# Kernel tuning notes

Measured on AMD Instinct MI355X. Metric: run time of the kernel, lower is better.

## Reference

```python
import jax, jax.numpy as jnp
import numpy as np


def cmul(a, b):
    # complex multiply on (..., 2) real/imag pairs
    ar, ai = a[..., 0], a[..., 1]
    br, bi = b[..., 0], b[..., 1]
    return jnp.stack([ar * br - ai * bi, ar * bi + ai * br], axis=-1)


def butterfly_apply(x, diag, subdiag, superdiag, k):
    # x: [B, n, 2]; tridiagonal-at-offset-k complex matrix applied to x.
    # diag: [n, 2]; subdiag/superdiag padded to [n, 2], first n-k entries used.
    n = x.shape[-2]
    out = cmul(diag, x)
    out = out.at[..., k:, :].add(cmul(subdiag[: n - k], x[..., : n - k, :]))
    out = out.at[..., : n - k, :].add(cmul(superdiag[: n - k], x[..., k:, :]))
    return out


def block_perm(x, logit, s):
    # Soft block permutation: within each contiguous block of size s,
    # mix identity with even-odd separation (prob p0), then mix each half
    # with its reversal (probs p1, p2). Acts identically on real & imag.
    B, n, _ = x.shape
    p = jax.nn.sigmoid(logit)
    y = x.reshape(B, n // s, s, 2)
    eo = jnp.concatenate([y[:, :, 0::2, :], y[:, :, 1::2, :]], axis=2)
    y = (1 - p[0]) * y + p[0] * eo
    h = s // 2
    first = (1 - p[1]) * y[:, :, :h, :] + p[1] * jnp.flip(y[:, :, :h, :], axis=2)
    second = (1 - p[2]) * y[:, :, h:, :] + p[2] * jnp.flip(y[:, :, h:, :], axis=2)
    return jnp.concatenate([first, second], axis=2).reshape(B, n, 2)


def trifat_forward(x, perm_logits, diags, subdiags, superdiags, bias):
    B, n = x.shape
    depth, m = diags.shape[0], diags.shape[1]
    perm_sizes = [n >> i for i in range(m - 1)][::-1]  # 4, 8, ..., n
    # real_to_complex: zero imaginary part
    xc = jnp.stack([x, jnp.zeros_like(x)], axis=-1)  # [B, n, 2]
    for d in range(depth):
        for j, s in enumerate(perm_sizes):
            xc = block_perm(xc, perm_logits[d, j], s)
        for i in range(m):
            k = n >> (i + 1)  # offsets n/2, n/4, ..., 1
            xc = butterfly_apply(xc, diags[d, i], subdiags[d, i], superdiags[d, i], k)
    return xc[..., 0] + bias  # take real part, add bias


def setup_inputs() -> dict:
    key = jax.random.key(0)
    ks = jax.random.split(key, 6)
    B, n, depth = 4096, 1024, 2
    m = int(np.log2(n))
    return {
        "x": jax.random.normal(ks[0], (B, n), jnp.float32),
        "perm_logits": jax.random.normal(ks[1], (depth, m - 1, 3), jnp.float32),
        "diags": jax.random.normal(ks[2], (depth, m, n, 2), jnp.float32),
        "subdiags": jax.random.normal(ks[3], (depth, m, n, 2), jnp.float32),
        "superdiags": jax.random.normal(ks[4], (depth, m, n, 2), jnp.float32),
        "bias": jnp.zeros((n,), jnp.float32),
    }


def reference(x, perm_logits, diags, subdiags, superdiags, bias):
    return trifat_forward(x, perm_logits, diags, subdiags, superdiags, bias)
```

## Files before the change

### kernel.cpp

```cpp
#include <hip/hip_runtime.h>

#define N 1024
#define THREADS 256
#define EPT 4

__device__ __forceinline__ float2* run_pipeline(
    float2* bufA, float2* bufB, int tid,
    const float* __restrict__ logits,
    const float* __restrict__ diags,
    const float* __restrict__ subd,
    const float* __restrict__ supd)
{
    float2* src = bufA;
    float2* dst = bufB;

    for (int d = 0; d < 2; ++d) {
        for (int j = 0; j < 9; ++j) {
            const int s = 4 << j;
            const int h = s >> 1;
            const float* lg = logits + (d * 9 + j) * 3;
            const float p0 = 1.0f / (1.0f + expf(-lg[0]));
            const float p1 = 1.0f / (1.0f + expf(-lg[1]));
            const float p2 = 1.0f / (1.0f + expf(-lg[2]));
#pragma unroll
            for (int e = 0; e < EPT; ++e) {
                const int idx = tid + e * THREADS;
                const int base = idx & ~(s - 1);
                const int t = idx & (s - 1);
                const bool lo = (t < h);

                const int eo_t = lo ? (2 * t) : (2 * (t - h) + 1);
                const float2 xt  = src[idx];
                const float2 xeo = src[base + eo_t];
                float2 yt;
                yt.x = xt.x + p0 * (xeo.x - xt.x);
                yt.y = xt.y + p0 * (xeo.y - xt.y);

                const int tm = lo ? (h - 1 - t) : (s + h - 1 - t);
                const float psel = lo ? p1 : p2;
                const int eo_m = (tm < h) ? (2 * tm) : (2 * (tm - h) + 1);
                const float2 xm   = src[base + tm];
                const float2 xmeo = src[base + eo_m];
                float2 ym;
                ym.x = xm.x + p0 * (xmeo.x - xm.x);
                ym.y = xm.y + p0 * (xmeo.y - xm.y);

                float2 o;
                o.x = yt.x + psel * (ym.x - yt.x);
                o.y = yt.y + psel * (ym.y - yt.y);
                dst[idx] = o;
            }
            __syncthreads();
            float2* tmp = src; src = dst; dst = tmp;
        }
        for (int i = 0; i < 10; ++i) {
            const int k = N >> (i + 1);
            const float2* Dg = (const float2*)(diags + (size_t)((d * 10 + i) * N) * 2);
            const float2* Sb = (const float2*)(subd  + (size_t)((d * 10 + i) * N) * 2);
            const float2* Sp = (const float2*)(supd  + (size_t)((d * 10 + i) * N) * 2);
#pragma unroll
            for (int e = 0; e < EPT; ++e) {
                const int idx = tid + e * THREADS;
                const float2 xv = src[idx];
                const float2 dg = Dg[idx];
                float2 o;
                o.x = dg.x * xv.x - dg.y * xv.y;
                o.y = dg.x * xv.y + dg.y * xv.x;
                if (idx >= k) {
                    const float2 xs = src[idx - k];
                    const float2 sb = Sb[idx - k];
                    o.x += sb.x * xs.x - sb.y * xs.y;
                    o.y += sb.x * xs.y + sb.y * xs.x;
                }
                if (idx < N - k) {
                    const float2 xp = src[idx + k];
                    const float2 sp = Sp[idx];
                    o.x += sp.x * xp.x - sp.y * xp.y;
                    o.y += sp.x * xp.y + sp.y * xp.x;
                }
                dst[idx] = o;
            }
            __syncthreads();
            float2* tmp = src; src = dst; dst = tmp;
        }
    }
    return src;
}

__global__ __launch_bounds__(THREADS) void trifat_kernel(
    const float* __restrict__ x,
    const float* __restrict__ logits,
    const float* __restrict__ diags,
    const float* __restrict__ supd_unused,
    const float* __restrict__ supd,
    const float* __restrict__ bias,
    float* __restrict__ out,
    int B);

__global__ __launch_bounds__(THREADS) void trifat_kernel_impl(
    const float* __restrict__ x,
    const float* __restrict__ logits,
    const float* __restrict__ diags,
    const float* __restrict__ subd,
    const float* __restrict__ supd,
    const float* __restrict__ bias,
    float* __restrict__ out,
    int B)
{
    __shared__ float2 bufA[N];
    __shared__ float2 bufB[N];

    const int row = blockIdx.x;
    const int tid = threadIdx.x;
    if (row >= B) return;

    const float* xr = x + (size_t)row * N;
#pragma unroll
    for (int e = 0; e < EPT; ++e) {
        int idx = tid + e * THREADS;
        bufA[idx] = make_float2(xr[idx], 0.0f);
    }
    __syncthreads();

    float2* res = run_pipeline(bufA, bufB, tid, logits, diags, subd, supd);

    float* orow = out + (size_t)row * N;
#pragma unroll
    for (int e = 0; e < EPT; ++e) {
        int idx = tid + e * THREADS;
        orow[idx] = res[idx].x + bias[idx];
    }
}

__device__ __forceinline__ unsigned short f2bf_rne(float f) {
    unsigned int u = __float_as_uint(f);
    unsigned int r = u + 0x7fffu + ((u >> 16) & 1u);
    return (unsigned short)(r >> 16);
}

#define TBW 512
#define NB_BUILD 512

__global__ __launch_bounds__(TBW) void prep_kernel(
    const float* __restrict__ logits,
    const float* __restrict__ diags,
    const float* __restrict__ subd,
    const float* __restrict__ supd,
    const float* __restrict__ x,
    unsigned short* __restrict__ Bt,
    unsigned short* __restrict__ A2)
{
    __shared__ __align__(16) float2 buf[2][2][N];

    const int tid = threadIdx.x;

    if (blockIdx.x >= NB_BUILD) {
        const int cb = blockIdx.x - NB_BUILD;
        const size_t base4 = (size_t)cb * 4096;
#pragma unroll
        for (int r = 0; r < 8; ++r) {
            const size_t g4 = base4 + r * 512 + tid;
            const float4 v = *(const float4*)(x + g4 * 4);
            ushort4 o;
            o.x = f2bf_rne(v.x);
            o.y = f2bf_rne(v.y);
            o.z = f2bf_rne(v.z);
            o.w = f2bf_rne(v.w);
            *(ushort4*)(A2 + g4 * 4) = o;
        }
        return;
    }

    const int j0 = blockIdx.x * 2;
    const int t = tid;

#pragma unroll
    for (int b = 0; b < 2; ++b)
#pragma unroll
        for (int v = 0; v < 2; ++v)
#pragma unroll
            for (int e = 0; e < 2; ++e)
                buf[b][v][tid + e * TBW] = make_float2(0.0f, 0.0f);
    __syncthreads();
    if (tid < 2) buf[0][tid][j0 + tid] = make_float2(1.0f, 0.0f);
    __syncthreads();

    int sb = 0;
    for (int d = 0; d < 2; ++d) {
        for (int jp = 0; jp < 9; ++jp) {
            const int s = 4 << jp;
            const int h = s >> 1;
            const int hh = s >> 2;
            const float* lg = logits + (d * 9 + jp) * 3;
            const float p0 = 1.0f / (1.0f + expf(-lg[0]));
            const float p1 = 1.0f / (1.0f + expf(-lg[1]));
            const float p2 = 1.0f / (1.0f + expf(-lg[2]));

            int w = -1, base = 0;
            if (d == 0) {
                if (tid < (s >> 1)) {
                    w = tid;
                    base = (j0 >> (jp + 2)) << (jp + 2);
                }
            } else {
                w = tid & ((s >> 1) - 1);
                base = (tid >> (jp + 1)) << (jp + 2);
            }

            if (w >= 0) {
                int tt, tm;
                float psel;
                if (w < hh) { tt = w;         tm = h - 1 - w;  psel = p1; }
                else        { const int u = w - hh; tt = h + u; tm = s - 1 - u; psel = p2; }

                const int eot = (tt < h) ? (2 * tt) : (2 * (tt - h) + 1);
                const int eom = (tm < h) ? (2 * tm) : (2 * (tm - h) + 1);

#pragma unroll
                for (int v = 0; v < 2; ++v) {
                    const float2* src = buf[sb][v];
                    float2* dst = buf[sb ^ 1][v];

                    const float2 xt = src[base + tt], xet = src[base + eot];
                    const float2 xm = src[base + tm], xem = src[base + eom];
                    float2 yt, ym;
                    yt.x = xt.x + p0 * (xet.x - xt.x);
                    yt.y = xt.y + p0 * (xet.y - xt.y);
                    ym.x = xm.x + p0 * (xem.x - xm.x);
                    ym.y = xm.y + p0 * (xem.y - xm.y);

                    float2 ot, om;
                    ot.x = yt.x + psel * (ym.x - yt.x);
                    ot.y = yt.y + psel * (ym.y - yt.y);
                    om.x = ym.x + psel * (yt.x - ym.x);
                    om.y = ym.y + psel * (yt.y - ym.y);
                    dst[base + tt] = ot;
                    dst[base + tm] = om;
                }
            }
            __syncthreads();
            sb ^= 1;
        }

        float4 dg4, sb4, sp4;
        {
            const float4* Dg4 = (const float4*)(diags + (size_t)((d * 10) * N) * 2);
            const float4* Sb4 = (const float4*)(subd  + (size_t)((d * 10) * N) * 2);
            const float4* Sp4 = (const float4*)(supd  + (size_t)((d * 10) * N) * 2);
            dg4 = Dg4[t];
            sb4 = (t >= 256) ? Sb4[t - 256] : make_float4(0.f, 0.f, 0.f, 0.f);
            sp4 = (t < 256)  ? Sp4[t]       : make_float4(0.f, 0.f, 0.f, 0.f);
        }
        for (int i = 0; i < 9; ++i) {
            const int k = N >> (i + 1);
            const int k2 = k >> 1;

            float4 dg4n, sb4n, sp4n;
            if (i < 8) {
                const int kn2 = k2 >> 1;
                const float4* Dg4 = (const float4*)(diags + (size_t)((d * 10 + i + 1) * N) * 2);
                const float4* Sb4 = (const float4*)(subd  + (size_t)((d * 10 + i + 1) * N) * 2);
                const float4* Sp4 = (const float4*)(supd  + (size_t)((d * 10 + i + 1) * N) * 2);
                dg4n = Dg4[t];
                sb4n = (t >= kn2)       ? Sb4[t - kn2] : make_float4(0.f, 0.f, 0.f, 0.f);
                sp4n = (t < 512 - kn2)  ? Sp4[t]       : make_float4(0.f, 0.f, 0.f, 0.f);
            }

            const bool has_sb = (t >= k2);
            const bool has_sp = (t < 512 - k2);
#pragma unroll
            for (int v = 0; v < 2; ++v) {
                const float2* src = buf[sb][v];
                const float4 xv = *(const float4*)(&src[2 * t]);
                float4 o;
                o.x = dg4.x * xv.x - dg4.y * xv.y;
                o.y = dg4.x * xv.y + dg4.y * xv.x;
                o.z = dg4.z * xv.z - dg4.w * xv.w;
                o.w = dg4.z * xv.w + dg4.w * xv.z;
                if (has_sb) {
                    const float4 xs = *(const float4*)(&src[2 * t - k]);
                    o.x += sb4.x * xs.x - sb4.y * xs.y;
                    o.y += sb4.x * xs.y + sb4.y * xs.x;
                    o.z += sb4.z * xs.z - sb4.w * xs.w;
                    o.w += sb4.z * xs.w + sb4.w * xs.z;
                }
                if (has_sp) {
                    const float4 xp = *(const float4*)(&src[2 * t + k]);
                    o.x += sp4.x * xp.x - sp4.y * xp.y;
                    o.y += sp4.x * xp.y + sp4.y * xp.x;
                    o.z += sp4.z * xp.z - sp4.w * xp.w;
                    o.w += sp4.z * xp.w + sp4.w * xp.z;
                }
                *(float4*)(&buf[sb ^ 1][v][2 * t]) = o;
            }
            __syncthreads();
            sb ^= 1;
            if (i < 8) { dg4 = dg4n; sb4 = sb4n; sp4 = sp4n; }
        }
        {
            const float2* Dg = (const float2*)(diags + (size_t)((d * 10 + 9) * N) * 2);
            const float2* Sb = (const float2*)(subd  + (size_t)((d * 10 + 9) * N) * 2);
            const float2* Sp = (const float2*)(supd  + (size_t)((d * 10 + 9) * N) * 2);
            const int i0 = 2 * t, i1 = 2 * t + 1;
            const float2 dg0 = Dg[i0], dg1 = Dg[i1];
            const float2 sb0 = (t >= 1) ? Sb[i0 - 1] : make_float2(0.f, 0.f);
            const float2 sb1 = Sb[i0];
            const float2 sp0 = Sp[i0];
            const float2 sp1 = (t < 511) ? Sp[i1] : make_float2(0.f, 0.f);
#pragma unroll
            for (int v = 0; v < 2; ++v) {
                const float2* src = buf[sb][v];
                const float2 x0 = src[i0], x1 = src[i1];
                float2 o0, o1;
                o0.x = dg0.x * x0.x - dg0.y * x0.y;
                o0.y = dg0.x * x0.y + dg0.y * x0.x;
                o1.x = dg1.x * x1.x - dg1.y * x1.y;
                o1.y = dg1.x * x1.y + dg1.y * x1.x;
                if (t >= 1) {
                    const float2 xs = src[i0 - 1];
                    o0.x += sb0.x * xs.x - sb0.y * xs.y;
                    o0.y += sb0.x * xs.y + sb0.y * xs.x;
                }
                o1.x += sb1.x * x0.x - sb1.y * x0.y;
                o1.y += sb1.x * x0.y + sb1.y * x0.x;
                o0.x += sp0.x * x1.x - sp0.y * x1.y;
                o0.y += sp0.x * x1.y + sp0.y * x1.x;
                if (t < 511) {
                    const float2 xp = src[i1 + 1];
                    o1.x += sp1.x * xp.x - sp1.y * xp.y;
                    o1.y += sp1.x * xp.y + sp1.y * xp.x;
                }
                float4 ow;
                ow.x = o0.x; ow.y = o0.y; ow.z = o1.x; ow.w = o1.y;
                *(float4*)(&buf[sb ^ 1][v][i0]) = ow;
            }
            __syncthreads();
            sb ^= 1;
        }
    }

#pragma unroll
    for (int v = 0; v < 2; ++v)
#pragma unroll
        for (int e = 0; e < 2; ++e) {
            const int idx = tid + e * TBW;
            Bt[(size_t)idx * N + (j0 + v)] = f2bf_rne(buf[sb][v][idx].x);
        }
}

typedef __attribute__((ext_vector_type(8))) __bf16 bf16x8;
typedef __attribute__((ext_vector_type(4))) float f32x4;

#define GLB(p) ((const __attribute__((address_space(1))) void*)(p))
#define LDS(p) ((__attribute__((address_space(3))) void*)(p))

__global__ __launch_bounds__(THREADS) void gemm_bf16(
    const unsigned short* __restrict__ A2,
    const unsigned short* __restrict__ Bt,
    const float* __restrict__ bias,
    float* __restrict__ out)
{
    __shared__ __align__(16) unsigned short As[128 * 64];
    __shared__ __align__(16) unsigned short Bs[64 * 64];

    const int m0 = blockIdx.x * 128;
    const int n0 = blockIdx.y * 64;
    const int tid = threadIdx.x;
    const int wave = tid >> 6, lane = tid & 63;
    const int wm = (wave >> 1) * 64, wn = (wave & 1) * 32;
    const int lrow = lane & 15, q = lane >> 4;
    const int r7 = lrow & 7;

    f32x4 acc[4][2] = {};

    for (int kt = 0; kt < 16; ++kt) {
        const int k0 = kt * 64;
        __syncthreads();
        {
            const unsigned short* gA = A2 + (size_t)m0 * N + k0;
            const unsigned short* gB = Bt + (size_t)n0 * N + k0;
#pragma unroll
            for (int r = 0; r < 4; ++r) {
                const int s = r * 256 + tid;
                const int row = s >> 3;
                const int gl = (s & 7) ^ (row & 7);
                __builtin_amdgcn_global_load_lds(GLB(gA + (size_t)row * N + gl * 8),
                                                 LDS(As + s * 8), 16, 0, 0);
            }
#pragma unroll
            for (int r = 0; r < 2; ++r) {
                const int s = r * 256 + tid;
                const int row = s >> 3;
                const int gl = (s & 7) ^ (row & 7);
                __builtin_amdgcn_global_load_lds(GLB(gB + (size_t)row * N + gl * 8),
                                                 LDS(Bs + s * 8), 16, 0, 0);
            }
        }
        __syncthreads();

#pragma unroll
        for (int kk = 0; kk < 64; kk += 32) {
            const int pg = ((kk >> 3) + q) ^ r7;
            bf16x8 a[4], b[2];
#pragma unroll
            for (int mi = 0; mi < 4; ++mi)
                a[mi] = *(const bf16x8*)(As + (wm + mi * 16 + lrow) * 64 + pg * 8);
#pragma unroll
            for (int ni = 0; ni < 2; ++ni)
                b[ni] = *(const bf16x8*)(Bs + (wn + ni * 16 + lrow) * 64 + pg * 8);
#pragma unroll
            for (int mi = 0; mi < 4; ++mi)
#pragma unroll
                for (int ni = 0; ni < 2; ++ni)
                    acc[mi][ni] = __builtin_amdgcn_mfma_f32_16x16x32_bf16(
                        a[mi], b[ni], acc[mi][ni], 0, 0, 0);
        }
    }

#pragma unroll
    for (int ni = 0; ni < 2; ++ni) {
        const int col = n0 + wn + ni * 16 + lrow;
        const float bv = bias[col];
#pragma unroll
        for (int mi = 0; mi < 4; ++mi)
#pragma unroll
            for (int r = 0; r < 4; ++r) {
                const int row = m0 + wm + mi * 16 + q * 4 + r;
                out[(size_t)row * N + col] = acc[mi][ni][r] + bv;
            }
    }
}

extern "C" void kernel_launch(void* const* d_in, const int* in_sizes, int n_in,
                              void* d_out, int out_size, void* d_ws, size_t ws_size,
                              hipStream_t stream) {
    const float* x      = (const float*)d_in[0];
    const float* logits = (const float*)d_in[1];
    const float* diags  = (const float*)d_in[2];
    const float* subd   = (const float*)d_in[3];
    const float* supd   = (const float*)d_in[4];
    const float* bias   = (const float*)d_in[5];
    float* out = (float*)d_out;

    const int B = in_sizes[0] / N;

    const size_t off_Bt = 0;
    const size_t off_A2 = 2u * 1024 * 1024;
    const size_t need   = off_A2 + (size_t)B * N * 2;

    if (ws_size >= need && B == 4096) {
        unsigned short* Bt = (unsigned short*)((char*)d_ws + off_Bt);
        unsigned short* A2 = (unsigned short*)((char*)d_ws + off_A2);

        prep_kernel<<<dim3(NB_BUILD + 256), dim3(TBW), 0, stream>>>(
            logits, diags, subd, supd, x, Bt, A2);
        gemm_bf16<<<dim3(B / 128, 16), dim3(THREADS), 0, stream>>>(A2, Bt, bias, out);
    } else {
        trifat_kernel_impl<<<dim3(B), dim3(THREADS), 0, stream>>>(
            x, logits, diags, subd, supd, bias, out, B);
    }
}
```

Baseline: 125.5 us.

## Give each wavefront its own basis column in prep kernel, replacing block barriers

The matrix-building prep kernel now assigns one basis column to each 64-lane wavefront, with four columns per 256-thread block, instead of two columns shared across a 512-thread block. Because each wavefront works only on its own LDS slice, every stage boundary uses a wave-local lgkmcnt wait plus a scheduling barrier instead of __syncthreads. Each lane now handles 8 tasks per stage, and the diagonal coefficients are reloaded per lane rather than prefetched. This relies on lockstep execution within a wavefront for LDS ordering, and it repeats coefficient loads per wave.

```diff
diff --git a/kernel.cpp b/kernel.cpp
--- a/kernel.cpp
+++ b/kernel.cpp
@@ -87,16 +87,6 @@
     return src;
 }
 
-__global__ __launch_bounds__(THREADS) void trifat_kernel(
-    const float* __restrict__ x,
-    const float* __restrict__ logits,
-    const float* __restrict__ diags,
-    const float* __restrict__ supd_unused,
-    const float* __restrict__ supd,
-    const float* __restrict__ bias,
-    float* __restrict__ out,
-    int B);
-
 __global__ __launch_bounds__(THREADS) void trifat_kernel_impl(
     const float* __restrict__ x,
     const float* __restrict__ logits,
@@ -138,10 +128,15 @@
     return (unsigned short)(r >> 16);
 }
 
-#define TBW 512
-#define NB_BUILD 512
-
-__global__ __launch_bounds__(TBW) void prep_kernel(
+#define LGKM0() do { \
+    asm volatile("s_waitcnt lgkmcnt(0)" ::: "memory"); \
+    __builtin_amdgcn_sched_barrier(0); \
+} while (0)
+
+#define TPW 256
+#define NBW 256
+
+__global__ __launch_bounds__(TPW) void prep_kernel(
     const float* __restrict__ logits,
     const float* __restrict__ diags,
     const float* __restrict__ subd,
@@ -150,16 +145,16 @@
     unsigned short* __restrict__ Bt,
     unsigned short* __restrict__ A2)
 {
-    __shared__ __align__(16) float2 buf[2][2][N];
+    __shared__ __align__(16) float2 buf[2][4][N];
 
     const int tid = threadIdx.x;
 
-    if (blockIdx.x >= NB_BUILD) {
-        const int cb = blockIdx.x - NB_BUILD;
+    if (blockIdx.x >= NBW) {
+        const int cb = blockIdx.x - NBW;
         const size_t base4 = (size_t)cb * 4096;
 #pragma unroll
-        for (int r = 0; r < 8; ++r) {
-            const size_t g4 = base4 + r * 512 + tid;
+        for (int r = 0; r < 16; ++r) {
+            const size_t g4 = base4 + (size_t)r * TPW + tid;
             const float4 v = *(const float4*)(x + g4 * 4);
             ushort4 o;
             o.x = f2bf_rne(v.x);
@@ -171,19 +166,18 @@
         return;
     }
 
-    const int j0 = blockIdx.x * 2;
-    const int t = tid;
+    const int lane = tid & 63;
+    const int w = tid >> 6;
+    const int j = blockIdx.x * 4 + w;
 
 #pragma unroll
     for (int b = 0; b < 2; ++b)
 #pragma unroll
-        for (int v = 0; v < 2; ++v)
-#pragma unroll
-            for (int e = 0; e < 2; ++e)
-                buf[b][v][tid + e * TBW] = make_float2(0.0f, 0.0f);
-    __syncthreads();
-    if (tid < 2) buf[0][tid][j0 + tid] = make_float2(1.0f, 0.0f);
-    __syncthreads();
+        for (int e = 0; e < 8; ++e)
+            *(float4*)(&buf[b][w][2 * (lane + 64 * e)]) = make_float4(0.f, 0.f, 0.f, 0.f);
+    LGKM0();
+    if (lane == 0) buf[0][w][j] = make_float2(1.0f, 0.0f);
+    LGKM0();
 
     int sb = 0;
     for (int d = 0; d < 2; ++d) {
@@ -192,124 +186,116 @@
             const int h = s >> 1;
             const int hh = s >> 2;
             const float* lg = logits + (d * 9 + jp) * 3;
-            const float p0 = 1.0f / (1.0f + expf(-lg[0]));
-            const float p1 = 1.0f / (1.0f + expf(-lg[1]));
-            const float p2 = 1.0f / (1.0f + expf(-lg[2]));
-
-            int w = -1, base = 0;
-            if (d == 0) {
-                if (tid < (s >> 1)) {
-                    w = tid;
-                    base = (j0 >> (jp + 2)) << (jp + 2);
-                }
-            } else {
-                w = tid & ((s >> 1) - 1);
-                base = (tid >> (jp + 1)) << (jp + 2);
-            }
-
-            if (w >= 0) {
+            const float p0 = 1.0f / (1.0f + __expf(-lg[0]));
+            const float p1 = 1.0f / (1.0f + __expf(-lg[1]));
+            const float p2 = 1.0f / (1.0f + __expf(-lg[2]));
+            const float2* src = buf[sb][w];
+            float2* dst = buf[sb ^ 1][w];
+
+            auto permTask = [&](int wt, int base) {
                 int tt, tm;
                 float psel;
-                if (w < hh) { tt = w;         tm = h - 1 - w;  psel = p1; }
-                else        { const int u = w - hh; tt = h + u; tm = s - 1 - u; psel = p2; }
+                if (wt < hh) { tt = wt;              tm = h - 1 - wt;  psel = p1; }
+                else         { const int u = wt - hh; tt = h + u; tm = s - 1 - u; psel = p2; }
 
                 const int eot = (tt < h) ? (2 * tt) : (2 * (tt - h) + 1);
                 const int eom = (tm < h) ? (2 * tm) : (2 * (tm - h) + 1);
 
-#pragma unroll
-                for (int v = 0; v < 2; ++v) {
-                    const float2* src = buf[sb][v];
-                    float2* dst = buf[sb ^ 1][v];
-
-                    const float2 xt = src[base + tt], xet = src[base + eot];
-                    const float2 xm = src[base + tm], xem = src[base + eom];
-                    float2 yt, ym;
-                    yt.x = xt.x + p0 * (xet.x - xt.x);
-                    yt.y = xt.y + p0 * (xet.y - xt.y);
-                    ym.x = xm.x + p0 * (xem.x - xm.x);
-                    ym.y = xm.y + p0 * (xem.y - xm.y);
-
-                    float2 ot, om;
-                    ot.x = yt.x + psel * (ym.x - yt.x);
-                    ot.y = yt.y + psel * (ym.y - yt.y);
-                    om.x = ym.x + psel * (yt.x - ym.x);
-                    om.y = ym.y + psel * (yt.y - ym.y);
-                    dst[base + tt] = ot;
-                    dst[base + tm] = om;
-                }
-            }
-            __syncthreads();
+                const float2 xt = src[base + tt], xet = src[base + eot];
+                const float2 xm = src[base + tm], xem = src[base + eom];
+                float2 yt, ym;
+                yt.x = xt.x + p0 * (xet.x - xt.x);
+                yt.y = xt.y + p0 * (xet.y - xt.y);
+                ym.x = xm.x + p0 * (xem.x - xm.x);
+                ym.y = xm.y + p0 * (xem.y - xm.y);
+
+                float2 ot, om;
+                ot.x = yt.x + psel * (ym.x - yt.x);
+                ot.y = yt.y + psel * (ym.y - yt.y);
+                om.x = ym.x + psel * (yt.x - ym.x);
+                om.y = ym.y + psel * (yt.y - ym.y);
+                dst[base + tt] = ot;
+                dst[base + tm] = om;
+            };
+
+            if (d == 0) {
+                const int base = (j >> (jp + 2)) << (jp + 2);
+#pragma unroll
+                for (int q = 0; q < 8; ++q) {
+                    const int task = lane + 64 * q;
+                    if (task < h) permTask(task, base);
+                }
+            } else {
+#pragma unroll
+                for (int q = 0; q < 8; ++q) {
+                    const int task = lane + 64 * q;
+                    permTask(task & (h - 1), (task >> (jp + 1)) << (jp + 2));
+                }
+            }
+            LGKM0();
             sb ^= 1;
         }
 
-        float4 dg4, sb4, sp4;
-        {
-            const float4* Dg4 = (const float4*)(diags + (size_t)((d * 10) * N) * 2);
-            const float4* Sb4 = (const float4*)(subd  + (size_t)((d * 10) * N) * 2);
-            const float4* Sp4 = (const float4*)(supd  + (size_t)((d * 10) * N) * 2);
-            dg4 = Dg4[t];
-            sb4 = (t >= 256) ? Sb4[t - 256] : make_float4(0.f, 0.f, 0.f, 0.f);
-            sp4 = (t < 256)  ? Sp4[t]       : make_float4(0.f, 0.f, 0.f, 0.f);
-        }
         for (int i = 0; i < 9; ++i) {
             const int k = N >> (i + 1);
             const int k2 = k >> 1;
-
-            float4 dg4n, sb4n, sp4n;
-            if (i < 8) {
-                const int kn2 = k2 >> 1;
-                const float4* Dg4 = (const float4*)(diags + (size_t)((d * 10 + i + 1) * N) * 2);
-                const float4* Sb4 = (const float4*)(subd  + (size_t)((d * 10 + i + 1) * N) * 2);
-                const float4* Sp4 = (const float4*)(supd  + (size_t)((d * 10 + i + 1) * N) * 2);
-                dg4n = Dg4[t];
-                sb4n = (t >= kn2)       ? Sb4[t - kn2] : make_float4(0.f, 0.f, 0.f, 0.f);
-                sp4n = (t < 512 - kn2)  ? Sp4[t]       : make_float4(0.f, 0.f, 0.f, 0.f);
-            }
-
-            const bool has_sb = (t >= k2);
-            const bool has_sp = (t < 512 - k2);
-#pragma unroll
-            for (int v = 0; v < 2; ++v) {
-                const float2* src = buf[sb][v];
-                const float4 xv = *(const float4*)(&src[2 * t]);
+            const float4* Dg4 = (const float4*)(diags + (size_t)((d * 10 + i) * N) * 2);
+            const float4* Sb4 = (const float4*)(subd  + (size_t)((d * 10 + i) * N) * 2);
+            const float4* Sp4 = (const float4*)(supd  + (size_t)((d * 10 + i) * N) * 2);
+            const float2* src = buf[sb][w];
+            float2* dst = buf[sb ^ 1][w];
+
+#pragma unroll
+            for (int e = 0; e < 8; ++e) {
+                const int g = lane + 64 * e;
+                const bool has_sb = (g >= k2);
+                const bool has_sp = (g < 512 - k2);
+                const float4 dg4 = Dg4[g];
+                const float4 sb4 = has_sb ? Sb4[g - k2] : make_float4(0.f, 0.f, 0.f, 0.f);
+                const float4 sp4 = has_sp ? Sp4[g]      : make_float4(0.f, 0.f, 0.f, 0.f);
+
+                const float4 xv = *(const float4*)(&src[2 * g]);
                 float4 o;
                 o.x = dg4.x * xv.x - dg4.y * xv.y;
                 o.y = dg4.x * xv.y + dg4.y * xv.x;
                 o.z = dg4.z * xv.z - dg4.w * xv.w;
                 o.w = dg4.z * xv.w + dg4.w * xv.z;
                 if (has_sb) {
-                    const float4 xs = *(const float4*)(&src[2 * t - k]);
+                    const float4 xs = *(const float4*)(&src[2 * g - k]);
                     o.x += sb4.x * xs.x - sb4.y * xs.y;
                     o.y += sb4.x * xs.y + sb4.y * xs.x;
                     o.z += sb4.z * xs.z - sb4.w * xs.w;
                     o.w += sb4.z * xs.w + sb4.w * xs.z;
                 }
                 if (has_sp) {
-                    const float4 xp = *(const float4*)(&src[2 * t + k]);
+                    const float4 xp = *(const float4*)(&src[2 * g + k]);
                     o.x += sp4.x * xp.x - sp4.y * xp.y;
                     o.y += sp4.x * xp.y + sp4.y * xp.x;
                     o.z += sp4.z * xp.z - sp4.w * xp.w;
                     o.w += sp4.z * xp.w + sp4.w * xp.z;
                 }
-                *(float4*)(&buf[sb ^ 1][v][2 * t]) = o;
-            }
-            __syncthreads();
+                *(float4*)(&dst[2 * g]) = o;
+            }
+            LGKM0();
             sb ^= 1;
-            if (i < 8) { dg4 = dg4n; sb4 = sb4n; sp4 = sp4n; }
         }
         {
             const float2* Dg = (const float2*)(diags + (size_t)((d * 10 + 9) * N) * 2);
             const float2* Sb = (const float2*)(subd  + (size_t)((d * 10 + 9) * N) * 2);
             const float2* Sp = (const float2*)(supd  + (size_t)((d * 10 + 9) * N) * 2);
-            const int i0 = 2 * t, i1 = 2 * t + 1;
-            const float2 dg0 = Dg[i0], dg1 = Dg[i1];
-            const float2 sb0 = (t >= 1) ? Sb[i0 - 1] : make_float2(0.f, 0.f);
-            const float2 sb1 = Sb[i0];
-            const float2 sp0 = Sp[i0];
-            const float2 sp1 = (t < 511) ? Sp[i1] : make_float2(0.f, 0.f);
-#pragma unroll
-            for (int v = 0; v < 2; ++v) {
-                const float2* src = buf[sb][v];
+            const float2* src = buf[sb][w];
+            float2* dst = buf[sb ^ 1][w];
+
+#pragma unroll
+            for (int e = 0; e < 8; ++e) {
+                const int t = lane + 64 * e;
+                const int i0 = 2 * t, i1 = 2 * t + 1;
+                const float2 dg0 = Dg[i0], dg1 = Dg[i1];
+                const float2 sb0 = (t >= 1)  ? Sb[i0 - 1] : make_float2(0.f, 0.f);
+                const float2 sb1 = Sb[i0];
+                const float2 sp0 = Sp[i0];
+                const float2 sp1 = (t < 511) ? Sp[i1]     : make_float2(0.f, 0.f);
+
                 const float2 x0 = src[i0], x1 = src[i1];
                 float2 o0, o1;
                 o0.x = dg0.x * x0.x - dg0.y * x0.y;
@@ -332,20 +318,18 @@
                 }
                 float4 ow;
                 ow.x = o0.x; ow.y = o0.y; ow.z = o1.x; ow.w = o1.y;
-                *(float4*)(&buf[sb ^ 1][v][i0]) = ow;
-            }
-            __syncthreads();
+                *(float4*)(&dst[i0]) = ow;
+            }
+            LGKM0();
             sb ^= 1;
         }
     }
 
 #pragma unroll
-    for (int v = 0; v < 2; ++v)
-#pragma unroll
-        for (int e = 0; e < 2; ++e) {
-            const int idx = tid + e * TBW;
-            Bt[(size_t)idx * N + (j0 + v)] = f2bf_rne(buf[sb][v][idx].x);
-        }
+    for (int e = 0; e < 16; ++e) {
+        const int idx = lane + 64 * e;
+        Bt[(size_t)idx * N + j] = f2bf_rne(buf[sb][w][idx].x);
+    }
 }
 
 typedef __attribute__((ext_vector_type(8))) __bf16 bf16x8;
@@ -452,7 +436,7 @@
         unsigned short* Bt = (unsigned short*)((char*)d_ws + off_Bt);
         unsigned short* A2 = (unsigned short*)((char*)d_ws + off_A2);
 
-        prep_kernel<<<dim3(NB_BUILD + 256), dim3(TBW), 0, stream>>>(
+        prep_kernel<<<dim3(NBW + 256), dim3(TPW), 0, stream>>>(
             logits, diags, subd, supd, x, Bt, A2);
         gemm_bf16<<<dim3(B / 128, 16), dim3(THREADS), 0, stream>>>(A2, Bt, bias, out);
     } else {
```

Result: slower. 175.5 us (+39.9%).
